# Optimization experiments

Hardware: AMD Instinct MI355X
Metric: run time of the kernel (lower is better)

Reference implementation:

```python
import jax, jax.numpy as jnp
import numpy as np
from jax import lax

DN = ('NCHW', 'OIHW', 'NCHW')


def setup_inputs() -> dict:
    key = jax.random.key(0)
    k1, k2, k3 = jax.random.split(key, 3)
    B, C, H, W = 16, 128, 64, 64
    hid, ker = 128, 3
    x = jax.random.normal(k1, (B, C, H, W), dtype=jnp.float32)
    # input-to-state masked conv: (4*hid, C, 1, ker)
    W_is = jax.random.normal(k2, (4 * hid, C, 1, ker), dtype=jnp.float32) * 0.02
    b_is = jnp.zeros((4 * hid,), dtype=jnp.float32)
    # state-to-state conv: (4*hid, hid, 1, ker)
    W_ss = jax.random.normal(k3, (4 * hid, hid, 1, ker), dtype=jnp.float32) * 0.02
    b_ss = jnp.zeros((4 * hid,), dtype=jnp.float32)
    return {"x": x, "W_is": W_is, "b_is": b_is, "W_ss": W_ss, "b_ss": b_ss}


def reference(x, W_is, b_is, W_ss, b_ss):
    B, C, H, W = x.shape
    hid = W_ss.shape[1]
    ker = W_is.shape[-1]
    pad = ker // 2

    # mask type 'B' on a (1, ker) kernel: keep columns <= center, zero to the right
    col_mask = (jnp.arange(ker) <= pad).astype(x.dtype)  # [ker]
    Wm = W_is * col_mask  # broadcast over (O, I, 1, ker)

    # input-to-state conv over the whole image once: [B, 4*hid, H, W]
    z_is = lax.conv_general_dilated(x, Wm, (1, 1), [(0, 0), (pad, pad)],
                                    dimension_numbers=DN) + b_is[None, :, None, None]

    h0 = jnp.zeros((B, hid, W), dtype=x.dtype)
    c0 = jnp.zeros((B, hid, W), dtype=x.dtype)

    def step(carry, z_row):
        h, c = carry  # [B, hid, W]
        z_ss = lax.conv_general_dilated(h[:, :, None, :], W_ss, (1, 1),
                                        [(0, 0), (pad, pad)],
                                        dimension_numbers=DN)[:, :, 0, :]
        z = z_row + z_ss + b_ss[None, :, None]  # [B, 4*hid, W]
        i_g = jax.nn.sigmoid(z[:, 0 * hid:1 * hid])
        f_g = jax.nn.sigmoid(z[:, 1 * hid:2 * hid])
        o_g = jax.nn.sigmoid(z[:, 2 * hid:3 * hid])
        g = jnp.tanh(z[:, 3 * hid:4 * hid])
        c = f_g * c + i_g * g
        h = o_g * jnp.tanh(c)
        return (h, c), h

    z_rows = jnp.moveaxis(z_is, 2, 0)  # [H, B, 4*hid, W]
    _, outs = lax.scan(step, (h0, c0), z_rows)  # outs: [H, B, hid, W]
    return jnp.moveaxis(outs, 0, 2)  # [B, hid, H, W]
```

## Files before the change

kernel.cpp:

```cpp
#include <hip/hip_runtime.h>
#include <math.h>

#define CIN    128
#define HID    128
#define HDIM   64
#define WDIM   64
#define HW     4096
#define KTOT   640
#define NTOT   512
#define LDSROW 136
#define NBATCH 16
#define BFRAG  (4 * 20 * 64 * 8)
#define HBUF   (NBATCH * WDIM * HID)

typedef short short8 __attribute__((ext_vector_type(8)));
typedef float f32x4  __attribute__((ext_vector_type(4)));
typedef unsigned int u32x4 __attribute__((ext_vector_type(4)));

#define ALOAD(p)     __hip_atomic_load((p), __ATOMIC_RELAXED, __HIP_MEMORY_SCOPE_AGENT)
#define ASTORE(p, v) __hip_atomic_store((p), (v), __ATOMIC_RELAXED, __HIP_MEMORY_SCOPE_AGENT)

__device__ __forceinline__ unsigned short f2bf(float f) {
    union { float f; unsigned int u; } v; v.f = f;
    unsigned int r = v.u + 0x7fffu + ((v.u >> 16) & 1u);
    return (unsigned short)(r >> 16);
}
__device__ __forceinline__ float sigm(float x)  { return 1.0f / (1.0f + __expf(-x)); }
__device__ __forceinline__ float tanhft(float x){ return 2.0f / (1.0f + __expf(-2.0f * x)) - 1.0f; }

__global__ void pack_kernel(const float* __restrict__ W_is,
                            const float* __restrict__ b_is,
                            const float* __restrict__ W_ss,
                            const float* __restrict__ b_ss,
                            unsigned short* __restrict__ Wpk,
                            float* __restrict__ bias_p,
                            unsigned int* __restrict__ bar) {
    int idx = blockIdx.x * blockDim.x + threadIdx.x;
    if (idx < NTOT * KTOT) {
        int j    = idx & 7;
        int lane = (idx >> 3) & 63;
        int t2   = idx >> 9;
        int ks   = t2 % 20;
        int gg   = t2 / 20;
        int g    = gg & 3;
        int he   = gg >> 2;
        int n = g * 128 + he * 16 + (lane & 15);
        int k = ks * 32 + (lane >> 4) * 8 + j;
        float v;
        if (k < 256) { int t = k >> 7, c = k & 127; v = W_is[((size_t)n * CIN + c) * 3 + t]; }
        else { int kk = k - 256; int t = kk >> 7, c = kk & 127; v = W_ss[((size_t)n * HID + c) * 3 + t]; }
        Wpk[idx] = f2bf(v);
    }
    if (idx < NTOT) bias_p[idx] = b_is[idx] + b_ss[idx];
    if (idx < NBATCH * HDIM) bar[idx] = 0;
}

#define GEMM_X(BUF)                                                            \
    {                                                                          \
        _Pragma("unroll")                                                      \
        for (int ks = 0; ks < 8; ++ks) {                                       \
            const int t = ks >> 2, c0 = (ks & 3) * 32;                         \
            short8 a = *(const short8*)&(BUF)[(wv * 16 + t) * LDSROW + c0 + a_off]; \
            _Pragma("unroll")                                                  \
            for (int g = 0; g < 4; ++g) {                                      \
                short8 bq = *(const short8*)&lds_b[((g * 20 + ks) * 64 + lane) * 8]; \
                acc[g] = __builtin_amdgcn_mfma_f32_16x16x32_bf16(a, bq, acc[g], 0, 0, 0); \
            }                                                                  \
        }                                                                      \
    }

#define GEMM_H(LDSH)                                                           \
    {                                                                          \
        _Pragma("unroll")                                                      \
        for (int ks = 0; ks < 12; ++ks) {                                      \
            const int t = ks >> 2, c0 = (ks & 3) * 32;                         \
            short8 a = *(const short8*)&(LDSH)[(wv * 16 + t) * LDSROW + c0 + a_off]; \
            _Pragma("unroll")                                                  \
            for (int g = 0; g < 4; ++g) {                                      \
                short8 bq = *(const short8*)&lds_b[((g * 20 + 8 + ks) * 64 + lane) * 8]; \
                acc[g] = __builtin_amdgcn_mfma_f32_16x16x32_bf16(a, bq, acc[g], 0, 0, 0); \
            }                                                                  \
        }                                                                      \
    }

#define STAGE_X(ROW, BUF)                                                      \
    {                                                                          \
        const float* xrow = x + (size_t)b * (CIN * HW) + (size_t)(ROW) * WDIM; \
        _Pragma("unroll")                                                      \
        for (int p = 0; p < 16; ++p) {                                         \
            int flat = p * 256 + tid;                                          \
            int w  = flat & 63;                                                \
            int cp = flat >> 6;                                                \
            float v0 = xrow[(2 * cp    ) * HW + w];                            \
            float v1 = xrow[(2 * cp + 1) * HW + w];                            \
            ((unsigned*)(BUF))[(w + 1) * 68 + cp] =                            \
                (unsigned)f2bf(v0) | ((unsigned)f2bf(v1) << 16);               \
        }                                                                      \
    }

#define STAGE_H_WAVE(HB, LDSH)                                                 \
    {                                                                          \
        const unsigned* hsrc = (const unsigned*)((HB) + (size_t)b * (WDIM * HID)); \
        unsigned hv_[18];                                                      \
        _Pragma("unroll")                                                      \
        for (int i = 0; i < 18; ++i) {                                         \
            int rr = wv * 16 - 1 + i;                                          \
            hv_[i] = (rr >= 0 && rr < 64) ? ALOAD(&hsrc[rr * 64 + lane]) : 0u; \
        }                                                                      \
        _Pragma("unroll")                                                      \
        for (int i = 0; i < 18; ++i) {                                         \
            int rr = wv * 16 - 1 + i;                                          \
            ((unsigned*)(LDSH))[(rr + 1) * 68 + lane] = hv_[i];                \
        }                                                                      \
    }

__global__ __launch_bounds__(256, 1) void lstm_kernel(
        const float* __restrict__ x,
        const unsigned short* __restrict__ Wpk,
        const float* __restrict__ bias_p,
        unsigned short* h_bf,
        unsigned int* bar,
        float* __restrict__ out) {
    __shared__ __align__(16) unsigned short lds_b[BFRAG];
    __shared__ __align__(16) unsigned short lds_x[2][66 * LDSROW];
    __shared__ __align__(16) unsigned short lds_h[2][66 * LDSROW];

    const int tid  = threadIdx.x;
    const int b    = blockIdx.x & 15;
    const int he   = blockIdx.x >> 4;
    const int wv   = tid >> 6;
    const int lane = tid & 63;
    const int quad = lane >> 4;
    const int l15  = lane & 15;

    {
        const u32x4* src = (const u32x4*)(Wpk + (size_t)he * BFRAG);
        u32x4* dst = (u32x4*)lds_b;
#pragma unroll
        for (int p = 0; p < 20; ++p) dst[p * 256 + tid] = src[p * 256 + tid];
    }
    if (tid < 68) {
        ((unsigned*)lds_x[0])[tid] = 0;
        ((unsigned*)lds_x[1])[tid] = 0;
        ((unsigned*)lds_h[0])[tid] = 0;
        ((unsigned*)lds_h[1])[tid] = 0;
        ((unsigned*)lds_h[0])[65 * 68 + tid] = 0;
        ((unsigned*)lds_h[1])[65 * 68 + tid] = 0;
    }
    STAGE_X(0, lds_x[0]);
    __syncthreads();

    const int hch = he * 16 + l15;
    const float bi  = bias_p[      hch];
    const float bf_ = bias_p[128 + hch];
    const float bo  = bias_p[256 + hch];
    const float bg  = bias_p[384 + hch];
    const int a_off = l15 * LDSROW + quad * 8;

    f32x4 acc[4];
#pragma unroll
    for (int g = 0; g < 4; ++g) acc[g] = (f32x4){0.f, 0.f, 0.f, 0.f};
    f32x4 creg = (f32x4){0.f, 0.f, 0.f, 0.f};

    GEMM_X(lds_x[0]);

    for (int r = 0; r < HDIM; ++r) {
        if (r < HDIM - 1) STAGE_X(r + 1, lds_x[(r + 1) & 1]);

        if (r > 0) {
            const int par = (r - 1) & 1;
            const unsigned* bp = &bar[(b << 6) + (r - 1)];
            while (ALOAD(bp) < 32u) { }
            STAGE_H_WAVE(h_bf + (size_t)par * HBUF, lds_h[par]);
            GEMM_H(lds_h[par]);
        }

        {
            const int w0 = wv * 16 + quad * 4;
            f32x4 hv;
#pragma unroll
            for (int e = 0; e < 4; ++e) {
                float zi = acc[0][e] + bi;
                float zf = acc[1][e] + bf_;
                float zo = acc[2][e] + bo;
                float zg = acc[3][e] + bg;
                float ig = sigm(zi), fg = sigm(zf), og = sigm(zo);
                float gg = tanhft(zg);
                float cn = fg * creg[e] + ig * gg;
                creg[e] = cn;
                hv[e]   = og * tanhft(cn);
            }
            *(f32x4*)&out[(((size_t)b * HID + hch) * HDIM + r) * WDIM + w0] = hv;
            unsigned short* hb = h_bf + (size_t)(r & 1) * HBUF
                               + ((size_t)b * WDIM + w0) * HID + hch;
#pragma unroll
            for (int e = 0; e < 4; ++e) ASTORE(&hb[e * HID], f2bf(hv[e]));
        }

        if (r < HDIM - 1) {
            asm volatile("s_waitcnt vmcnt(0) lgkmcnt(0)" ::: "memory");
            if (lane == 0)
                __hip_atomic_fetch_add(&bar[(b << 6) + r], 1u,
                                       __ATOMIC_RELAXED, __HIP_MEMORY_SCOPE_AGENT);
            __syncthreads();
#pragma unroll
            for (int g = 0; g < 4; ++g) acc[g] = (f32x4){0.f, 0.f, 0.f, 0.f};
            GEMM_X(lds_x[(r + 1) & 1]);
        }
    }
}

extern "C" void kernel_launch(void* const* d_in, const int* in_sizes, int n_in,
                              void* d_out, int out_size, void* d_ws, size_t ws_size,
                              hipStream_t stream) {
    const float* x    = (const float*)d_in[0];
    const float* W_is = (const float*)d_in[1];
    const float* b_is = (const float*)d_in[2];
    const float* W_ss = (const float*)d_in[3];
    const float* b_ss = (const float*)d_in[4];
    float* out = (float*)d_out;

    unsigned short* h_bf   = (unsigned short*)d_ws;
    unsigned short* Wpk    = (unsigned short*)((char*)d_ws + 524288);
    float*          bias_p = (float*)((char*)d_ws + 1179648);
    unsigned int*   bar    = (unsigned int*)((char*)d_ws + 1181696);

    pack_kernel<<<(NTOT * KTOT + 255) / 256, 256, 0, stream>>>(
        W_is, b_is, W_ss, b_ss, Wpk, bias_p, bar);
    lstm_kernel<<<128, 256, 0, stream>>>(x, Wpk, bias_p, h_bf, bar, out);
}
```

Baseline: 386.6 us.

## Precompute input GEMM in parallel kernel and replace barrier with tagged h polling

Hoists the input-to-state convolution GEMM out of the serial recurrence into a separate, fully parallel kernel that writes pre-activations to a 128MB workspace buffer, which the recurrent kernel reads each row. It also replaces the per-row atomic counter barrier with sequence-tagged h values: each 32-bit word packs the bf16 hidden value with the row index, and consumers poll until every tag matches. This removes the waitcnt, atomic add and counter spin from the critical path. The cost is extra HBM traffic for z, added polling loads, and a fallback path when the workspace is too small.

Result: slower. 447.2 us (+15.7%).

```diff
diff --git a/kernel.cpp b/kernel.cpp
--- a/kernel.cpp
+++ b/kernel.cpp
@@ -6,12 +6,12 @@
 #define HDIM   64
 #define WDIM   64
 #define HW     4096
-#define KTOT   640
 #define NTOT   512
 #define LDSROW 136
 #define NBATCH 16
-#define BFRAG  (4 * 20 * 64 * 8)
-#define HBUF   (NBATCH * WDIM * HID)
+#define WXSZ   (4 * 8 * 64 * 8)
+#define WHSZ   (4 * 12 * 64 * 8)
+#define HTWORDS (2 * NBATCH * WDIM * HID)
 
 typedef short short8 __attribute__((ext_vector_type(8)));
 typedef float f32x4  __attribute__((ext_vector_type(4)));
@@ -19,6 +19,9 @@
 
 #define ALOAD(p)     __hip_atomic_load((p), __ATOMIC_RELAXED, __HIP_MEMORY_SCOPE_AGENT)
 #define ASTORE(p, v) __hip_atomic_store((p), (v), __ATOMIC_RELAXED, __HIP_MEMORY_SCOPE_AGENT)
+
+#define Z_IDX(b_, he_, r_, wv_, g_, lane_) \
+    ((((((((size_t)(b_) * 8 + (he_)) * 64 + (r_)) * 4 + (wv_)) * 4 + (g_)) * 64) + (lane_)) * 4)
 
 __device__ __forceinline__ unsigned short f2bf(float f) {
     union { float f; unsigned int u; } v; v.f = f;
@@ -32,56 +35,28 @@
                             const float* __restrict__ b_is,
                             const float* __restrict__ W_ss,
                             const float* __restrict__ b_ss,
-                            unsigned short* __restrict__ Wpk,
+                            unsigned short* __restrict__ Wx,
+                            unsigned short* __restrict__ Wh,
                             float* __restrict__ bias_p,
-                            unsigned int* __restrict__ bar) {
+                            unsigned int* __restrict__ ht) {
     int idx = blockIdx.x * blockDim.x + threadIdx.x;
-    if (idx < NTOT * KTOT) {
-        int j    = idx & 7;
-        int lane = (idx >> 3) & 63;
-        int t2   = idx >> 9;
-        int ks   = t2 % 20;
-        int gg   = t2 / 20;
-        int g    = gg & 3;
-        int he   = gg >> 2;
+    if (idx < 131072) {
+        int j = idx & 7, lane = (idx >> 3) & 63, rest = idx >> 9;
+        int ks = rest & 7, gg = rest >> 3, g = gg & 3, he = gg >> 2;
         int n = g * 128 + he * 16 + (lane & 15);
-        int k = ks * 32 + (lane >> 4) * 8 + j;
-        float v;
-        if (k < 256) { int t = k >> 7, c = k & 127; v = W_is[((size_t)n * CIN + c) * 3 + t]; }
-        else { int kk = k - 256; int t = kk >> 7, c = kk & 127; v = W_ss[((size_t)n * HID + c) * 3 + t]; }
-        Wpk[idx] = f2bf(v);
+        int k = ks * 32 + ((lane >> 4) * 8) + j;
+        Wx[idx] = f2bf(W_is[((size_t)n * CIN + (k & 127)) * 3 + (k >> 7)]);
+    }
+    if (idx < 196608) {
+        int j = idx & 7, lane = (idx >> 3) & 63, rest = idx >> 9;
+        int ks = rest % 12, gg = rest / 12, g = gg & 3, he = gg >> 2;
+        int n = g * 128 + he * 16 + (lane & 15);
+        int k = ks * 32 + ((lane >> 4) * 8) + j;
+        Wh[idx] = f2bf(W_ss[((size_t)n * HID + (k & 127)) * 3 + (k >> 7)]);
     }
     if (idx < NTOT) bias_p[idx] = b_is[idx] + b_ss[idx];
-    if (idx < NBATCH * HDIM) bar[idx] = 0;
-}
-
-#define GEMM_X(BUF)                                                            \
-    {                                                                          \
-        _Pragma("unroll")                                                      \
-        for (int ks = 0; ks < 8; ++ks) {                                       \
-            const int t = ks >> 2, c0 = (ks & 3) * 32;                         \
-            short8 a = *(const short8*)&(BUF)[(wv * 16 + t) * LDSROW + c0 + a_off]; \
-            _Pragma("unroll")                                                  \
-            for (int g = 0; g < 4; ++g) {                                      \
-                short8 bq = *(const short8*)&lds_b[((g * 20 + ks) * 64 + lane) * 8]; \
-                acc[g] = __builtin_amdgcn_mfma_f32_16x16x32_bf16(a, bq, acc[g], 0, 0, 0); \
-            }                                                                  \
-        }                                                                      \
-    }
-
-#define GEMM_H(LDSH)                                                           \
-    {                                                                          \
-        _Pragma("unroll")                                                      \
-        for (int ks = 0; ks < 12; ++ks) {                                      \
-            const int t = ks >> 2, c0 = (ks & 3) * 32;                         \
-            short8 a = *(const short8*)&(LDSH)[(wv * 16 + t) * LDSROW + c0 + a_off]; \
-            _Pragma("unroll")                                                  \
-            for (int g = 0; g < 4; ++g) {                                      \
-                short8 bq = *(const short8*)&lds_b[((g * 20 + 8 + ks) * 64 + lane) * 8]; \
-                acc[g] = __builtin_amdgcn_mfma_f32_16x16x32_bf16(a, bq, acc[g], 0, 0, 0); \
-            }                                                                  \
-        }                                                                      \
-    }
+    if (idx < HTWORDS) ht[idx] = 0u;
+}
 
 #define STAGE_X(ROW, BUF)                                                      \
     {                                                                          \
@@ -98,32 +73,114 @@
         }                                                                      \
     }
 
-#define STAGE_H_WAVE(HB, LDSH)                                                 \
+#define GEMM_X(BUF)                                                            \
     {                                                                          \
-        const unsigned* hsrc = (const unsigned*)((HB) + (size_t)b * (WDIM * HID)); \
-        unsigned hv_[18];                                                      \
+        _Pragma("unroll")                                                      \
+        for (int ks = 0; ks < 8; ++ks) {                                       \
+            const int t = ks >> 2, c0 = (ks & 3) * 32;                         \
+            short8 a = *(const short8*)&(BUF)[(wv * 16 + t) * LDSROW + c0 + a_off]; \
+            _Pragma("unroll")                                                  \
+            for (int g = 0; g < 4; ++g) {                                      \
+                short8 bq = *(const short8*)&lds_bx[((g * 8 + ks) * 64 + lane) * 8]; \
+                acc[g] = __builtin_amdgcn_mfma_f32_16x16x32_bf16(a, bq, acc[g], 0, 0, 0); \
+            }                                                                  \
+        }                                                                      \
+    }
+
+#define GEMM_H(LDSH)                                                           \
+    {                                                                          \
+        _Pragma("unroll")                                                      \
+        for (int ks = 0; ks < 12; ++ks) {                                      \
+            const int t = ks >> 2, c0 = (ks & 3) * 32;                         \
+            short8 a = *(const short8*)&(LDSH)[(wv * 16 + t) * LDSROW + c0 + a_off]; \
+            _Pragma("unroll")                                                  \
+            for (int g = 0; g < 4; ++g) {                                      \
+                short8 bq = *(const short8*)&lds_bh[((g * 12 + ks) * 64 + lane) * 8]; \
+                acc[g] = __builtin_amdgcn_mfma_f32_16x16x32_bf16(a, bq, acc[g], 0, 0, 0); \
+            }                                                                  \
+        }                                                                      \
+    }
+
+#define POLL_H(PAR, WANT, LDSH)                                                \
+    {                                                                          \
+        const unsigned* hs = ht + ((size_t)(PAR) * NBATCH + b) * (WDIM * HID); \
+        unsigned a_[18], b_[18];                                               \
+        const int base = wv * 16 - 1;                                          \
+        for (;;) {                                                             \
+            unsigned diff = 0;                                                 \
+            _Pragma("unroll")                                                  \
+            for (int i = 0; i < 18; ++i) {                                     \
+                int rr = base + i;                                             \
+                unsigned va, vb;                                               \
+                if ((unsigned)rr < 64u) {                                      \
+                    const unsigned* p = hs + rr * 128 + 2 * lane;              \
+                    va = ALOAD(p); vb = ALOAD(p + 1);                          \
+                } else { va = vb = (unsigned)(WANT); }                         \
+                a_[i] = va; b_[i] = vb;                                        \
+                diff |= ((va ^ (unsigned)(WANT)) | (vb ^ (unsigned)(WANT))) & 0xffffu; \
+            }                                                                  \
+            if (__ballot(diff != 0u) == 0ull) break;                           \
+        }                                                                      \
         _Pragma("unroll")                                                      \
         for (int i = 0; i < 18; ++i) {                                         \
-            int rr = wv * 16 - 1 + i;                                          \
-            hv_[i] = (rr >= 0 && rr < 64) ? ALOAD(&hsrc[rr * 64 + lane]) : 0u; \
-        }                                                                      \
-        _Pragma("unroll")                                                      \
-        for (int i = 0; i < 18; ++i) {                                         \
-            int rr = wv * 16 - 1 + i;                                          \
-            ((unsigned*)(LDSH))[(rr + 1) * 68 + lane] = hv_[i];                \
-        }                                                                      \
-    }
-
+            int rr = base + i;                                                 \
+            ((unsigned*)(LDSH))[(rr + 1) * 68 + lane] =                        \
+                (a_[i] >> 16) | (b_[i] & 0xffff0000u);                         \
+        }                                                                      \
+    }
+
+__global__ __launch_bounds__(256) void xgemm_kernel(
+        const float* __restrict__ x,
+        const unsigned short* __restrict__ Wx,
+        float* __restrict__ z) {
+    __shared__ __align__(16) unsigned short lds_bx[WXSZ];
+    __shared__ __align__(16) unsigned short ldsx[2][66 * LDSROW];
+
+    const int tid  = threadIdx.x;
+    const int b    = blockIdx.x & 15;
+    const int he   = (blockIdx.x >> 4) & 7;
+    const int rg   = blockIdx.x >> 7;
+    const int wv   = tid >> 6;
+    const int lane = tid & 63;
+    const int quad = lane >> 4;
+    const int l15  = lane & 15;
+    const int a_off = l15 * LDSROW + quad * 8;
+
+    {
+        const u32x4* src = (const u32x4*)(Wx + (size_t)he * WXSZ);
+        u32x4* dst = (u32x4*)lds_bx;
+#pragma unroll
+        for (int p = 0; p < 8; ++p) dst[p * 256 + tid] = src[p * 256 + tid];
+    }
+    if (tid < 68) { ((unsigned*)ldsx[0])[tid] = 0; ((unsigned*)ldsx[1])[tid] = 0; }
+
+    for (int rr = 0; rr < 8; ++rr) {
+        const int r = rg * 8 + rr;
+        STAGE_X(r, ldsx[rr & 1]);
+        __syncthreads();
+        f32x4 acc[4];
+#pragma unroll
+        for (int g = 0; g < 4; ++g) acc[g] = (f32x4){0.f, 0.f, 0.f, 0.f};
+        GEMM_X(ldsx[rr & 1]);
+#pragma unroll
+        for (int g = 0; g < 4; ++g)
+            *(f32x4*)(z + Z_IDX(b, he, r, wv, g, lane)) = acc[g];
+    }
+}
+
+template <bool USE_Z>
 __global__ __launch_bounds__(256, 1) void lstm_kernel(
         const float* __restrict__ x,
-        const unsigned short* __restrict__ Wpk,
+        const unsigned short* __restrict__ Wx,
+        const unsigned short* __restrict__ Wh,
         const float* __restrict__ bias_p,
-        unsigned short* h_bf,
-        unsigned int* bar,
+        const float* __restrict__ z,
+        unsigned int* ht,
         float* __restrict__ out) {
-    __shared__ __align__(16) unsigned short lds_b[BFRAG];
-    __shared__ __align__(16) unsigned short lds_x[2][66 * LDSROW];
-    __shared__ __align__(16) unsigned short lds_h[2][66 * LDSROW];
+    __shared__ __align__(16) unsigned short lds_bh[WHSZ];
+    __shared__ __align__(16) unsigned short lds_bx[USE_Z ? 16 : WXSZ];
+    __shared__ __align__(16) unsigned short ldsx[2][USE_Z ? 16 : 66 * LDSROW];
+    __shared__ __align__(16) unsigned short ldsh[2][66 * LDSROW];
 
     const int tid  = threadIdx.x;
     const int b    = blockIdx.x & 15;
@@ -132,22 +189,22 @@
     const int lane = tid & 63;
     const int quad = lane >> 4;
     const int l15  = lane & 15;
+    const int a_off = l15 * LDSROW + quad * 8;
 
     {
-        const u32x4* src = (const u32x4*)(Wpk + (size_t)he * BFRAG);
-        u32x4* dst = (u32x4*)lds_b;
-#pragma unroll
-        for (int p = 0; p < 20; ++p) dst[p * 256 + tid] = src[p * 256 + tid];
-    }
-    if (tid < 68) {
-        ((unsigned*)lds_x[0])[tid] = 0;
-        ((unsigned*)lds_x[1])[tid] = 0;
-        ((unsigned*)lds_h[0])[tid] = 0;
-        ((unsigned*)lds_h[1])[tid] = 0;
-        ((unsigned*)lds_h[0])[65 * 68 + tid] = 0;
-        ((unsigned*)lds_h[1])[65 * 68 + tid] = 0;
-    }
-    STAGE_X(0, lds_x[0]);
+        const u32x4* src = (const u32x4*)(Wh + (size_t)he * WHSZ);
+        u32x4* dst = (u32x4*)lds_bh;
+#pragma unroll
+        for (int p = 0; p < 12; ++p) dst[p * 256 + tid] = src[p * 256 + tid];
+    }
+    if constexpr (!USE_Z) {
+        const u32x4* src = (const u32x4*)(Wx + (size_t)he * WXSZ);
+        u32x4* dst = (u32x4*)lds_bx;
+#pragma unroll
+        for (int p = 0; p < 8; ++p) dst[p * 256 + tid] = src[p * 256 + tid];
+        if (tid < 68) { ((unsigned*)ldsx[0])[tid] = 0; ((unsigned*)ldsx[1])[tid] = 0; }
+        STAGE_X(0, ldsx[0]);
+    }
     __syncthreads();
 
     const int hch = he * 16 + l15;
@@ -155,24 +212,30 @@
     const float bf_ = bias_p[128 + hch];
     const float bo  = bias_p[256 + hch];
     const float bg  = bias_p[384 + hch];
-    const int a_off = l15 * LDSROW + quad * 8;
 
     f32x4 acc[4];
 #pragma unroll
     for (int g = 0; g < 4; ++g) acc[g] = (f32x4){0.f, 0.f, 0.f, 0.f};
     f32x4 creg = (f32x4){0.f, 0.f, 0.f, 0.f};
-
-    GEMM_X(lds_x[0]);
+    f32x4 zx[4];
+
+    if constexpr (!USE_Z) GEMM_X(ldsx[0]);
 
     for (int r = 0; r < HDIM; ++r) {
-        if (r < HDIM - 1) STAGE_X(r + 1, lds_x[(r + 1) & 1]);
+        if constexpr (USE_Z) {
+            const float* zb = z + Z_IDX(b, he, r, wv, 0, lane);
+#pragma unroll
+            for (int g = 0; g < 4; ++g) zx[g] = *(const f32x4*)(zb + g * 256);
+#pragma unroll
+            for (int g = 0; g < 4; ++g) acc[g] = (f32x4){0.f, 0.f, 0.f, 0.f};
+        } else {
+            if (r < HDIM - 1) STAGE_X(r + 1, ldsx[(r + 1) & 1]);
+        }
 
         if (r > 0) {
             const int par = (r - 1) & 1;
-            const unsigned* bp = &bar[(b << 6) + (r - 1)];
-            while (ALOAD(bp) < 32u) { }
-            STAGE_H_WAVE(h_bf + (size_t)par * HBUF, lds_h[par]);
-            GEMM_H(lds_h[par]);
+            POLL_H(par, r, ldsh[par]);
+            GEMM_H(ldsh[par]);
         }
 
         {
@@ -180,32 +243,39 @@
             f32x4 hv;
 #pragma unroll
             for (int e = 0; e < 4; ++e) {
-                float zi = acc[0][e] + bi;
-                float zf = acc[1][e] + bf_;
-                float zo = acc[2][e] + bo;
-                float zg = acc[3][e] + bg;
+                float zi, zf, zo, zg;
+                if constexpr (USE_Z) {
+                    zi = zx[0][e] + acc[0][e] + bi;
+                    zf = zx[1][e] + acc[1][e] + bf_;
+                    zo = zx[2][e] + acc[2][e] + bo;
+                    zg = zx[3][e] + acc[3][e] + bg;
+                } else {
+                    zi = acc[0][e] + bi;
+                    zf = acc[1][e] + bf_;
+                    zo = acc[2][e] + bo;
+                    zg = acc[3][e] + bg;
+                }
                 float ig = sigm(zi), fg = sigm(zf), og = sigm(zo);
                 float gg = tanhft(zg);
                 float cn = fg * creg[e] + ig * gg;
                 creg[e] = cn;
                 hv[e]   = og * tanhft(cn);
             }
+            unsigned* hb = ht + ((size_t)(r & 1) * NBATCH + b) * (WDIM * HID);
+#pragma unroll
+            for (int e = 0; e < 4; ++e)
+                ASTORE(&hb[(w0 + e) * 128 + hch],
+                       ((unsigned)f2bf(hv[e]) << 16) | (unsigned)(r + 1));
             *(f32x4*)&out[(((size_t)b * HID + hch) * HDIM + r) * WDIM + w0] = hv;
-            unsigned short* hb = h_bf + (size_t)(r & 1) * HBUF
-                               + ((size_t)b * WDIM + w0) * HID + hch;
-#pragma unroll
-            for (int e = 0; e < 4; ++e) ASTORE(&hb[e * HID], f2bf(hv[e]));
         }
 
-        if (r < HDIM - 1) {
-            asm volatile("s_waitcnt vmcnt(0) lgkmcnt(0)" ::: "memory");
-            if (lane == 0)
-                __hip_atomic_fetch_add(&bar[(b << 6) + r], 1u,
-                                       __ATOMIC_RELAXED, __HIP_MEMORY_SCOPE_AGENT);
-            __syncthreads();
-#pragma unroll
-            for (int g = 0; g < 4; ++g) acc[g] = (f32x4){0.f, 0.f, 0.f, 0.f};
-            GEMM_X(lds_x[(r + 1) & 1]);
+        if constexpr (!USE_Z) {
+            if (r < HDIM - 1) {
+                __syncthreads();
+#pragma unroll
+                for (int g = 0; g < 4; ++g) acc[g] = (f32x4){0.f, 0.f, 0.f, 0.f};
+                GEMM_X(ldsx[(r + 1) & 1]);
+            }
         }
     }
 }
@@ -220,12 +290,29 @@
     const float* b_ss = (const float*)d_in[4];
     float* out = (float*)d_out;
 
-    unsigned short* h_bf   = (unsigned short*)d_ws;
-    unsigned short* Wpk    = (unsigned short*)((char*)d_ws + 524288);
-    float*          bias_p = (float*)((char*)d_ws + 1179648);
-    unsigned int*   bar    = (unsigned int*)((char*)d_ws + 1181696);
-
-    pack_kernel<<<(NTOT * KTOT + 255) / 256, 256, 0, stream>>>(
-        W_is, b_is, W_ss, b_ss, Wpk, bias_p, bar);
-    lstm_kernel<<<128, 256, 0, stream>>>(x, Wpk, bias_p, h_bf, bar, out);
-}
+    const size_t Z_BYTES  = (size_t)33554432 * 4;
+    const size_t HT_BYTES = (size_t)HTWORDS * 4;
+    const size_t WX_BYTES = 8 * WXSZ * 2;
+    const size_t WH_BYTES = 8 * WHSZ * 2;
+    const size_t need_z   = Z_BYTES + HT_BYTES + WX_BYTES + WH_BYTES + 2048;
+
+    if (ws_size >= need_z) {
+        float*          zbuf   = (float*)d_ws;
+        unsigned int*   ht     = (unsigned int*)((char*)d_ws + Z_BYTES);
+        unsigned short* Wx     = (unsigned short*)((char*)d_ws + Z_BYTES + HT_BYTES);
+        unsigned short* Wh     = (unsigned short*)((char*)d_ws + Z_BYTES + HT_BYTES + WX_BYTES);
+        float*          bias_p = (float*)((char*)d_ws + Z_BYTES + HT_BYTES + WX_BYTES + WH_BYTES);
+
+        pack_kernel<<<1024, 256, 0, stream>>>(W_is, b_is, W_ss, b_ss, Wx, Wh, bias_p, ht);
+        xgemm_kernel<<<1024, 256, 0, stream>>>(x, Wx, zbuf);
+        lstm_kernel<true><<<128, 256, 0, stream>>>(x, Wx, Wh, bias_p, zbuf, ht, out);
+    } else {
+        unsigned int*   ht     = (unsigned int*)d_ws;
+        unsigned short* Wx     = (unsigned short*)((char*)d_ws + HT_BYTES);
+        unsigned short* Wh     = (unsigned short*)((char*)d_ws + HT_BYTES + WX_BYTES);
+        float*          bias_p = (float*)((char*)d_ws + HT_BYTES + WX_BYTES + WH_BYTES);
+
+        pack_kernel<<<1024, 256, 0, stream>>>(W_is, b_is, W_ss, b_ss, Wx, Wh, bias_p, ht);
+        lstm_kernel<false><<<128, 256, 0, stream>>>(x, Wx, Wh, bias_p, (const float*)d_ws, ht, out);
+    }
+}
```
